# Kernel optimization log

Hardware: AMD Instinct MI355X
Metric: run time of the kernel (lower is better)

## Reference

```python
import jax, jax.numpy as jnp
import numpy as np

B, D_IN, UNITS = 8192, 4096, 4096

def setup_inputs() -> dict:
    key = jax.random.key(0)
    k1, k2 = jax.random.split(key)
    x = jax.random.normal(k1, (B, D_IN), dtype=jnp.float32)
    w = jax.random.normal(k2, (D_IN, UNITS), dtype=jnp.float32)
    b = jnp.zeros((UNITS,), dtype=jnp.float32)
    return {"x": x, "w": w, "b": b}

def reference(x, w, b):
    # Bipolar dense: sign-binarize the weights, full-precision matmul, bias, relu.
    weights = jnp.sign(w)  # values in {-1, 0, +1}; matches tf.math.sign
    out = jnp.matmul(x, weights) + b  # [B, UNITS]
    return jax.nn.relu(out)
```

## Files before the change

kernel.cpp:

```cpp
#include <hip/hip_runtime.h>
#include <hip/hip_bf16.h>
#include <stdint.h>

#define M_DIM 8192
#define N_DIM 4096
#define K_DIM 4096

typedef __attribute__((ext_vector_type(4))) int   int4v;
typedef __attribute__((ext_vector_type(4))) float floatx4;

__global__ __launch_bounds__(256) void quant_x_kernel(const float* __restrict__ x,
                                                      signed char* __restrict__ xq,
                                                      float* __restrict__ xs) {
    const int row = blockIdx.x;
    const int tid = threadIdx.x;
    const int wave = tid >> 6, lane = tid & 63;
    const float4* xr = (const float4*)(x + (size_t)row * K_DIM);

    float4 v[4];
    float m = 0.f;
    #pragma unroll
    for (int j = 0; j < 4; ++j) {
        v[j] = xr[j * 256 + tid];
        m = fmaxf(m, fmaxf(fmaxf(fabsf(v[j].x), fabsf(v[j].y)),
                           fmaxf(fabsf(v[j].z), fabsf(v[j].w))));
    }
    #pragma unroll
    for (int off = 32; off >= 1; off >>= 1) m = fmaxf(m, __shfl_down(m, off));
    __shared__ float wm_s[4];
    if (lane == 0) wm_s[wave] = m;
    __syncthreads();
    const float M = fmaxf(fmaxf(wm_s[0], wm_s[1]), fmaxf(wm_s[2], wm_s[3]));
    const float inv = M > 0.f ? 127.f / M : 0.f;
    if (tid == 0) xs[row] = M > 0.f ? M / 127.f : 0.f;

    char4* xo = (char4*)(xq + (size_t)row * K_DIM);
    #pragma unroll
    for (int j = 0; j < 4; ++j) {
        char4 q;
        q.x = (signed char)__float2int_rn(v[j].x * inv);
        q.y = (signed char)__float2int_rn(v[j].y * inv);
        q.z = (signed char)__float2int_rn(v[j].z * inv);
        q.w = (signed char)__float2int_rn(v[j].w * inv);
        xo[j * 256 + tid] = q;
    }
}

__global__ __launch_bounds__(256) void cvt_w_kernel(const float* __restrict__ w,
                                                    signed char* __restrict__ wT) {
    __shared__ signed char tile[64][68];
    const int t  = threadIdx.x;
    const int k0 = blockIdx.y * 64;
    const int n0 = blockIdx.x * 64;
    #pragma unroll
    for (int p = 0; p < 4; ++p) {
        int kk = p * 16 + (t >> 4);
        int nn = (t & 15) * 4;
        float4 v = *reinterpret_cast<const float4*>(&w[(size_t)(k0 + kk) * N_DIM + n0 + nn]);
        tile[kk][nn + 0] = v.x > 0.f ? 1 : (v.x < 0.f ? -1 : 0);
        tile[kk][nn + 1] = v.y > 0.f ? 1 : (v.y < 0.f ? -1 : 0);
        tile[kk][nn + 2] = v.z > 0.f ? 1 : (v.z < 0.f ? -1 : 0);
        tile[kk][nn + 3] = v.w > 0.f ? 1 : (v.w < 0.f ? -1 : 0);
    }
    __syncthreads();
    const int r = t >> 2;
    const int c = (t & 3) * 16;
    int4v o;
    signed char* op = (signed char*)&o;
    #pragma unroll
    for (int j = 0; j < 16; ++j) op[j] = tile[c + j][r];
    *reinterpret_cast<int4v*>(&wT[(size_t)(n0 + r) * K_DIM + k0 + c]) = o;
}

#define BM 256
#define BN 256
#define BK 64
#define NT (K_DIM / BK)

#define GLD(gsrc, ldst) __builtin_amdgcn_global_load_lds( \
    (const __attribute__((address_space(1))) unsigned int*)(gsrc), \
    (__attribute__((address_space(3))) unsigned int*)(ldst), 16, 0, 0)

__global__ __launch_bounds__(512, 2) void gemm_i8_kernel(
    const signed char* __restrict__ A,
    const signed char* __restrict__ BT,
    const float* __restrict__ xsc,
    const float* __restrict__ bias,
    float* __restrict__ C)
{
    __shared__ signed char As[4][2][128 * 64];
    __shared__ signed char Bs[4][2][128 * 64];

    const int tid  = threadIdx.x;
    const int wave = tid >> 6;
    const int lane = tid & 63;
    const int wm   = wave >> 2;
    const int wn   = wave & 3;
    const int bh   = wn >> 1;
    const int brow0 = (wn & 1) * 64;

    const int bid  = blockIdx.x;
    const int sbid = (bid & 7) * 64 + (bid >> 3);
    const int tn   = sbid & 15;
    const int tm   = sbid >> 4;
    const int bm   = tm * BM;
    const int bn   = tn * BN;

    const int srow = tid >> 2;
    const int scol = ((tid & 3) ^ ((tid >> 3) & 3)) * 16;

    const int laneRow = (lane & 15) * 64;
    const int colX = ((lane >> 4) * 16) ^ (((lane >> 1) & 3) << 4);

    int4v acc[8][4] = {};

#define STAGE_HALF(G, R0, KOFS, LDST) do { \
    GLD((G) + (size_t)((R0) + srow) * K_DIM + (KOFS) + scol, (LDST) + wave * 1024); \
  } while (0)

#define STAGE_TILE(SLOT, KOFS) do { \
    STAGE_HALF(A,  bm,       (KOFS), As[SLOT][0]); \
    STAGE_HALF(A,  bm + 128, (KOFS), As[SLOT][1]); \
    STAGE_HALF(BT, bn,       (KOFS), Bs[SLOT][0]); \
    STAGE_HALF(BT, bn + 128, (KOFS), Bs[SLOT][1]); \
  } while (0)

#define READ_FRAGS(SLOT, FA, FA2, FB) do { \
    const char* Ar = (const char*)As[SLOT][wm]; \
    const char* Br = (const char*)Bs[SLOT][bh]; \
    FA[0]  = *(const int4v*)(Ar + (0*16)*64 + laneRow + colX); \
    FB[0]  = *(const int4v*)(Br + (brow0 +  0)*64 + laneRow + colX); \
    FB[1]  = *(const int4v*)(Br + (brow0 + 16)*64 + laneRow + colX); \
    FB[2]  = *(const int4v*)(Br + (brow0 + 32)*64 + laneRow + colX); \
    FB[3]  = *(const int4v*)(Br + (brow0 + 48)*64 + laneRow + colX); \
    FA[1]  = *(const int4v*)(Ar + (1*16)*64 + laneRow + colX); \
    FA[2]  = *(const int4v*)(Ar + (2*16)*64 + laneRow + colX); \
    FA[3]  = *(const int4v*)(Ar + (3*16)*64 + laneRow + colX); \
    FA2[0] = *(const int4v*)(Ar + ((64 + 0*16))*64 + laneRow + colX); \
    FA2[1] = *(const int4v*)(Ar + ((64 + 1*16))*64 + laneRow + colX); \
    FA2[2] = *(const int4v*)(Ar + ((64 + 2*16))*64 + laneRow + colX); \
    FA2[3] = *(const int4v*)(Ar + ((64 + 3*16))*64 + laneRow + colX); \
  } while (0)

#define MFMA_TILE(FA, FA2, FB) do { \
    __builtin_amdgcn_s_setprio(1); \
    _Pragma("unroll") \
    for (int mf = 0; mf < 4; ++mf) \
        _Pragma("unroll") \
        for (int nf = 0; nf < 4; ++nf) \
            acc[mf][nf] = __builtin_amdgcn_mfma_i32_16x16x64_i8( \
                FA[mf], FB[nf], acc[mf][nf], 0, 0, 0); \
    _Pragma("unroll") \
    for (int mf = 0; mf < 4; ++mf) \
        _Pragma("unroll") \
        for (int nf = 0; nf < 4; ++nf) \
            acc[4 + mf][nf] = __builtin_amdgcn_mfma_i32_16x16x64_i8( \
                FA2[mf], FB[nf], acc[4 + mf][nf], 0, 0, 0); \
    __builtin_amdgcn_s_setprio(0); \
  } while (0)

#define TILE_BODY(T, CA, CA2, CB, NA, NA2, NB) do { \
    const int kS = ((T) + 3 < NT ? (T) + 3 : NT - 1) * BK; \
    const int rs = ((T) + 1 < NT ? (T) + 1 : NT - 1) & 3; \
    STAGE_TILE(((T) + 3) & 3, kS); \
    READ_FRAGS(rs, NA, NA2, NB); \
    MFMA_TILE(CA, CA2, CB); \
    asm volatile("s_waitcnt vmcnt(4)" ::: "memory"); \
    __builtin_amdgcn_s_barrier(); \
  } while (0)

    STAGE_TILE(0, 0);
    STAGE_TILE(1, BK);
    STAGE_TILE(2, 2 * BK);
    asm volatile("s_waitcnt vmcnt(4)" ::: "memory");
    __builtin_amdgcn_s_barrier();

    int4v aA[4], a2A[4], bA[4];
    int4v aB[4], a2B[4], bB[4];
    READ_FRAGS(0, aA, a2A, bA);

    for (int t = 0; t < NT; t += 2) {
        TILE_BODY(t,     aA, a2A, bA, aB, a2B, bB);
        TILE_BODY(t + 1, aB, a2B, bB, aA, a2A, bA);
    }

    float bv[4];
    #pragma unroll
    for (int nf = 0; nf < 4; ++nf)
        bv[nf] = bias[bn + wn * 64 + nf * 16 + (lane & 15)];
    #pragma unroll
    for (int mf = 0; mf < 8; ++mf) {
        const int row0 = bm + wm * 128 + mf * 16 + (lane >> 4) * 4;
        float sr[4];
        #pragma unroll
        for (int r = 0; r < 4; ++r) sr[r] = xsc[row0 + r];
        #pragma unroll
        for (int nf = 0; nf < 4; ++nf) {
            const int col = bn + wn * 64 + nf * 16 + (lane & 15);
            float* cp = C + (size_t)row0 * N_DIM + col;
            #pragma unroll
            for (int r = 0; r < 4; ++r) {
                float v = (float)acc[mf][nf][r] * sr[r] + bv[nf];
                cp[(size_t)r * N_DIM] = v > 0.f ? v : 0.f;
            }
        }
    }
}

__global__ void naive_kernel(const float* __restrict__ x, const float* __restrict__ w,
                             const float* __restrict__ b, float* __restrict__ out) {
    __shared__ float xs[16][16];
    __shared__ float ws[16][17];
    const int row = blockIdx.y * 16 + threadIdx.y;
    const int col = blockIdx.x * 16 + threadIdx.x;
    float acc = 0.f;
    for (int k0 = 0; k0 < K_DIM; k0 += 16) {
        xs[threadIdx.y][threadIdx.x] = x[(size_t)row * K_DIM + k0 + threadIdx.x];
        float wv = w[(size_t)(k0 + threadIdx.y) * N_DIM + col];
        ws[threadIdx.y][threadIdx.x] = wv > 0.f ? 1.f : (wv < 0.f ? -1.f : 0.f);
        __syncthreads();
        #pragma unroll
        for (int kk = 0; kk < 16; ++kk) acc += xs[threadIdx.y][kk] * ws[kk][threadIdx.x];
        __syncthreads();
    }
    float v = acc + b[col];
    out[(size_t)row * N_DIM + col] = v > 0.f ? v : 0.f;
}

extern "C" void kernel_launch(void* const* d_in, const int* in_sizes, int n_in,
                              void* d_out, int out_size, void* d_ws, size_t ws_size,
                              hipStream_t stream) {
    const float* x = (const float*)d_in[0];
    const float* w = (const float*)d_in[1];
    const float* b = (const float*)d_in[2];
    float* out = (float*)d_out;

    const size_t xq_bytes = (size_t)M_DIM * K_DIM;
    const size_t wT_bytes = (size_t)K_DIM * N_DIM;
    const size_t xs_bytes = (size_t)M_DIM * sizeof(float);

    if (ws_size >= xq_bytes + wT_bytes + xs_bytes) {
        signed char* xq = (signed char*)d_ws;
        signed char* wT = (signed char*)((char*)d_ws + xq_bytes);
        float*       xs = (float*)((char*)d_ws + xq_bytes + wT_bytes);
        quant_x_kernel<<<M_DIM, 256, 0, stream>>>(x, xq, xs);
        cvt_w_kernel<<<dim3(N_DIM / 64, K_DIM / 64), 256, 0, stream>>>(w, wT);
        gemm_i8_kernel<<<(M_DIM / BM) * (N_DIM / BN), 512, 0, stream>>>(xq, wT, xs, b, out);
    } else {
        naive_kernel<<<dim3(N_DIM / 16, M_DIM / 16), dim3(16, 16), 0, stream>>>(x, w, b, out);
    }
}
```

Measured before the change: 216.1 us.

## Pre-pack B into MFMA fragment layout and load it directly to registers

The weight conversion kernel now writes the sign-binarized weights in a per-(64-column, 64-k) chunk layout that matches the MFMA B-fragment order. The GEMM then loads B fragments straight from global memory into registers, one tile ahead, instead of staging them through LDS. LDS drops to a 3-slot A-only buffer with a two-tile prefetch distance. This removes the B LDS traffic and footprint, but B reads become per-wave global loads whose latency must be hidden by the shallower register prefetch. A is also prefetched less deeply than before.

```diff
diff --git a/kernel.cpp b/kernel.cpp
--- a/kernel.cpp
+++ b/kernel.cpp
@@ -47,7 +47,7 @@
 }
 
 __global__ __launch_bounds__(256) void cvt_w_kernel(const float* __restrict__ w,
-                                                    signed char* __restrict__ wT) {
+                                                    signed char* __restrict__ Bf) {
     __shared__ signed char tile[64][68];
     const int t  = threadIdx.x;
     const int k0 = blockIdx.y * 64;
@@ -63,13 +63,15 @@
         tile[kk][nn + 3] = v.w > 0.f ? 1 : (v.w < 0.f ? -1 : 0);
     }
     __syncthreads();
-    const int r = t >> 2;
-    const int c = (t & 3) * 16;
+    const int nf   = t >> 6;
+    const int lane = t & 63;
     int4v o;
     signed char* op = (signed char*)&o;
     #pragma unroll
-    for (int j = 0; j < 16; ++j) op[j] = tile[c + j][r];
-    *reinterpret_cast<int4v*>(&wT[(size_t)(n0 + r) * K_DIM + k0 + c]) = o;
+    for (int j = 0; j < 16; ++j)
+        op[j] = tile[(lane >> 4) * 16 + j][nf * 16 + (lane & 15)];
+    const size_t chunk = ((size_t)blockIdx.x * (K_DIM / 64) + blockIdx.y) * 4096;
+    *reinterpret_cast<int4v*>(Bf + chunk + nf * 1024 + lane * 16) = o;
 }
 
 #define BM 256
@@ -83,21 +85,18 @@
 
 __global__ __launch_bounds__(512, 2) void gemm_i8_kernel(
     const signed char* __restrict__ A,
-    const signed char* __restrict__ BT,
+    const signed char* __restrict__ Bf,
     const float* __restrict__ xsc,
     const float* __restrict__ bias,
     float* __restrict__ C)
 {
-    __shared__ signed char As[4][2][128 * 64];
-    __shared__ signed char Bs[4][2][128 * 64];
+    __shared__ signed char As[3][256 * 64];
 
     const int tid  = threadIdx.x;
     const int wave = tid >> 6;
     const int lane = tid & 63;
     const int wm   = wave >> 2;
     const int wn   = wave & 3;
-    const int bh   = wn >> 1;
-    const int brow0 = (wn & 1) * 64;
 
     const int bid  = blockIdx.x;
     const int sbid = (bid & 7) * 64 + (bid >> 3);
@@ -111,77 +110,79 @@
 
     const int laneRow = (lane & 15) * 64;
     const int colX = ((lane >> 4) * 16) ^ (((lane >> 1) & 3) << 4);
+    const int Abase = wm * 128 * 64;
+
+    const signed char* bfb = Bf + ((size_t)((bn >> 6) + wn) * (K_DIM / 64)) * 4096
+                                + lane * 16;
 
     int4v acc[8][4] = {};
 
-#define STAGE_HALF(G, R0, KOFS, LDST) do { \
-    GLD((G) + (size_t)((R0) + srow) * K_DIM + (KOFS) + scol, (LDST) + wave * 1024); \
-  } while (0)
-
-#define STAGE_TILE(SLOT, KOFS) do { \
-    STAGE_HALF(A,  bm,       (KOFS), As[SLOT][0]); \
-    STAGE_HALF(A,  bm + 128, (KOFS), As[SLOT][1]); \
-    STAGE_HALF(BT, bn,       (KOFS), Bs[SLOT][0]); \
-    STAGE_HALF(BT, bn + 128, (KOFS), Bs[SLOT][1]); \
-  } while (0)
-
-#define READ_FRAGS(SLOT, FA, FA2, FB) do { \
-    const char* Ar = (const char*)As[SLOT][wm]; \
-    const char* Br = (const char*)Bs[SLOT][bh]; \
-    FA[0]  = *(const int4v*)(Ar + (0*16)*64 + laneRow + colX); \
-    FB[0]  = *(const int4v*)(Br + (brow0 +  0)*64 + laneRow + colX); \
-    FB[1]  = *(const int4v*)(Br + (brow0 + 16)*64 + laneRow + colX); \
-    FB[2]  = *(const int4v*)(Br + (brow0 + 32)*64 + laneRow + colX); \
-    FB[3]  = *(const int4v*)(Br + (brow0 + 48)*64 + laneRow + colX); \
-    FA[1]  = *(const int4v*)(Ar + (1*16)*64 + laneRow + colX); \
-    FA[2]  = *(const int4v*)(Ar + (2*16)*64 + laneRow + colX); \
-    FA[3]  = *(const int4v*)(Ar + (3*16)*64 + laneRow + colX); \
-    FA2[0] = *(const int4v*)(Ar + ((64 + 0*16))*64 + laneRow + colX); \
-    FA2[1] = *(const int4v*)(Ar + ((64 + 1*16))*64 + laneRow + colX); \
-    FA2[2] = *(const int4v*)(Ar + ((64 + 2*16))*64 + laneRow + colX); \
-    FA2[3] = *(const int4v*)(Ar + ((64 + 3*16))*64 + laneRow + colX); \
-  } while (0)
-
-#define MFMA_TILE(FA, FA2, FB) do { \
+#define STAGE_A(KOFS, SLOT) do { \
+    GLD(A + (size_t)(bm + srow) * K_DIM + (KOFS) + scol, As[SLOT] + wave * 1024); \
+    GLD(A + (size_t)(bm + 128 + srow) * K_DIM + (KOFS) + scol, \
+        As[SLOT] + 8192 + wave * 1024); \
+  } while (0)
+
+#define LOAD_B(SLOT, KT) do { \
+    const signed char* _b = bfb + (size_t)(KT) * 4096; \
+    SLOT[0] = *(const int4v*)(_b + 0 * 1024); \
+    SLOT[1] = *(const int4v*)(_b + 1 * 1024); \
+    SLOT[2] = *(const int4v*)(_b + 2 * 1024); \
+    SLOT[3] = *(const int4v*)(_b + 3 * 1024); \
+  } while (0)
+
+#define READ_A() do { \
+    a[0]  = *(const int4v*)(Ar + Abase + (0*16)*64 + laneRow + colX); \
+    a[1]  = *(const int4v*)(Ar + Abase + (1*16)*64 + laneRow + colX); \
+    a[2]  = *(const int4v*)(Ar + Abase + (2*16)*64 + laneRow + colX); \
+    a[3]  = *(const int4v*)(Ar + Abase + (3*16)*64 + laneRow + colX); \
+    a2[0] = *(const int4v*)(Ar + Abase + ((64+0*16))*64 + laneRow + colX); \
+    a2[1] = *(const int4v*)(Ar + Abase + ((64+1*16))*64 + laneRow + colX); \
+    a2[2] = *(const int4v*)(Ar + Abase + ((64+2*16))*64 + laneRow + colX); \
+    a2[3] = *(const int4v*)(Ar + Abase + ((64+3*16))*64 + laneRow + colX); \
+  } while (0)
+
+#define MFMA_T(BREG) do { \
     __builtin_amdgcn_s_setprio(1); \
     _Pragma("unroll") \
     for (int mf = 0; mf < 4; ++mf) \
         _Pragma("unroll") \
         for (int nf = 0; nf < 4; ++nf) \
             acc[mf][nf] = __builtin_amdgcn_mfma_i32_16x16x64_i8( \
-                FA[mf], FB[nf], acc[mf][nf], 0, 0, 0); \
+                a[mf], BREG[nf], acc[mf][nf], 0, 0, 0); \
     _Pragma("unroll") \
     for (int mf = 0; mf < 4; ++mf) \
         _Pragma("unroll") \
         for (int nf = 0; nf < 4; ++nf) \
             acc[4 + mf][nf] = __builtin_amdgcn_mfma_i32_16x16x64_i8( \
-                FA2[mf], FB[nf], acc[4 + mf][nf], 0, 0, 0); \
+                a2[mf], BREG[nf], acc[4 + mf][nf], 0, 0, 0); \
     __builtin_amdgcn_s_setprio(0); \
   } while (0)
 
-#define TILE_BODY(T, CA, CA2, CB, NA, NA2, NB) do { \
-    const int kS = ((T) + 3 < NT ? (T) + 3 : NT - 1) * BK; \
-    const int rs = ((T) + 1 < NT ? (T) + 1 : NT - 1) & 3; \
-    STAGE_TILE(((T) + 3) & 3, kS); \
-    READ_FRAGS(rs, NA, NA2, NB); \
-    MFMA_TILE(CA, CA2, CB); \
-    asm volatile("s_waitcnt vmcnt(4)" ::: "memory"); \
+#define TILE_BODY(T, BCUR, BNXT) do { \
+    const char* Ar = (const char*)As[(T) % 3]; \
+    const int kA = ((T) + 2 < NT ? (T) + 2 : NT - 1) * BK; \
+    const int kB = ((T) + 1 < NT ? (T) + 1 : NT - 1); \
+    STAGE_A(kA, ((T) + 2) % 3); \
+    LOAD_B(BNXT, kB); \
+    READ_A(); \
+    MFMA_T(BCUR); \
+    asm volatile("s_waitcnt vmcnt(6)" ::: "memory"); \
     __builtin_amdgcn_s_barrier(); \
   } while (0)
 
-    STAGE_TILE(0, 0);
-    STAGE_TILE(1, BK);
-    STAGE_TILE(2, 2 * BK);
-    asm volatile("s_waitcnt vmcnt(4)" ::: "memory");
+    STAGE_A(0,  0);
+    STAGE_A(BK, 1);
+    int4v bX[4], bY[4];
+    LOAD_B(bX, 0);
+    asm volatile("s_waitcnt vmcnt(0)" ::: "memory");
     __builtin_amdgcn_s_barrier();
 
-    int4v aA[4], a2A[4], bA[4];
-    int4v aB[4], a2B[4], bB[4];
-    READ_FRAGS(0, aA, a2A, bA);
+    int4v a[4], a2[4];
 
     for (int t = 0; t < NT; t += 2) {
-        TILE_BODY(t,     aA, a2A, bA, aB, a2B, bB);
-        TILE_BODY(t + 1, aB, a2B, bB, aA, a2A, bA);
+        TILE_BODY(t,     bX, bY);
+        TILE_BODY(t + 1, bY, bX);
     }
 
     float bv[4];
@@ -236,16 +237,16 @@
     float* out = (float*)d_out;
 
     const size_t xq_bytes = (size_t)M_DIM * K_DIM;
-    const size_t wT_bytes = (size_t)K_DIM * N_DIM;
+    const size_t bf_bytes = (size_t)K_DIM * N_DIM;
     const size_t xs_bytes = (size_t)M_DIM * sizeof(float);
 
-    if (ws_size >= xq_bytes + wT_bytes + xs_bytes) {
+    if (ws_size >= xq_bytes + bf_bytes + xs_bytes) {
         signed char* xq = (signed char*)d_ws;
-        signed char* wT = (signed char*)((char*)d_ws + xq_bytes);
-        float*       xs = (float*)((char*)d_ws + xq_bytes + wT_bytes);
+        signed char* Bf = (signed char*)((char*)d_ws + xq_bytes);
+        float*       xs = (float*)((char*)d_ws + xq_bytes + bf_bytes);
         quant_x_kernel<<<M_DIM, 256, 0, stream>>>(x, xq, xs);
-        cvt_w_kernel<<<dim3(N_DIM / 64, K_DIM / 64), 256, 0, stream>>>(w, wT);
-        gemm_i8_kernel<<<(M_DIM / BM) * (N_DIM / BN), 512, 0, stream>>>(xq, wT, xs, b, out);
+        cvt_w_kernel<<<dim3(N_DIM / 64, K_DIM / 64), 256, 0, stream>>>(w, Bf);
+        gemm_i8_kernel<<<(M_DIM / BM) * (N_DIM / BN), 512, 0, stream>>>(xq, Bf, xs, b, out);
     } else {
         naive_kernel<<<dim3(N_DIM / 16, M_DIM / 16), dim3(16, 16), 0, stream>>>(x, w, b, out);
     }
```

Result: faster. 198.4 us (-8.2%).
